# Kernel optimization log

Measured on AMD Instinct MI355X. Metric: run time of the kernel, lower is better.

The kernel has to match this reference:

```python
import jax, jax.numpy as jnp
import numpy as np

B, T = 32, 64
STOCH, DETER, HIDDEN = 1024, 4096, 1024
ACT_DIM, EMBED = 128, 1536
MIN_STD = 0.1
EPS = 1e-3  # dreamerv3-torch uses LayerNorm(eps=1e-3)


def _ln(x, g, b):
    m = jnp.mean(x, -1, keepdims=True)
    v = jnp.var(x, -1, keepdims=True)
    return (x - m) * jax.lax.rsqrt(v + EPS) * g + b


def setup_inputs() -> dict:
    key = jax.random.key(0)
    ks = jax.random.split(key, 24)

    def w(k, fan_in, fan_out):
        return jax.random.normal(k, (fan_in, fan_out), jnp.float32) / np.sqrt(fan_in)

    inp = {
        "embed": jax.random.normal(ks[0], (B, T, EMBED), jnp.float32),
        "action": jax.random.normal(ks[1], (B, T, ACT_DIM), jnp.float32),
        "is_first": jnp.zeros((B, T), jnp.bool_),
        "init_deter": jax.random.normal(ks[2], (B, DETER), jnp.float32),
        "init_stoch": jax.random.normal(ks[3], (B, STOCH), jnp.float32),
        "noise_prior": jax.random.normal(ks[4], (B, T, STOCH), jnp.float32),
        "noise_post": jax.random.normal(ks[5], (B, T, STOCH), jnp.float32),
        # _img_in_layers: Linear(stoch+act -> hidden, no bias) + LN + SiLU
        "W_in": w(ks[6], STOCH + ACT_DIM, HIDDEN),
        "g_in": 1.0 + 0.1 * jax.random.normal(ks[7], (HIDDEN,), jnp.float32),
        "b_in": 0.1 * jax.random.normal(ks[8], (HIDDEN,), jnp.float32),
        # GRUCell: Linear(hidden+deter -> 3*deter, no bias) + LN
        "W_gru": w(ks[9], HIDDEN + DETER, 3 * DETER),
        "g_gru": 1.0 + 0.1 * jax.random.normal(ks[10], (3 * DETER,), jnp.float32),
        "b_gru": 0.1 * jax.random.normal(ks[11], (3 * DETER,), jnp.float32),
        # _img_out_layers: Linear(deter -> hidden, no bias) + LN + SiLU
        "W_imgout": w(ks[12], DETER, HIDDEN),
        "g_io": 1.0 + 0.1 * jax.random.normal(ks[13], (HIDDEN,), jnp.float32),
        "b_io": 0.1 * jax.random.normal(ks[14], (HIDDEN,), jnp.float32),
        # _obs_out_layers: Linear(deter+embed -> hidden, no bias) + LN + SiLU
        "W_obsout": w(ks[15], DETER + EMBED, HIDDEN),
        "g_oo": 1.0 + 0.1 * jax.random.normal(ks[16], (HIDDEN,), jnp.float32),
        "b_oo": 0.1 * jax.random.normal(ks[17], (HIDDEN,), jnp.float32),
        # suff-stats layers: Linear(hidden -> 2*stoch) with bias
        "W_ims": w(ks[18], HIDDEN, 2 * STOCH),
        "b_ims": 0.01 * jax.random.normal(ks[19], (2 * STOCH,), jnp.float32),
        "W_obs": w(ks[20], HIDDEN, 2 * STOCH),
        "b_obs": 0.01 * jax.random.normal(ks[21], (2 * STOCH,), jnp.float32),
    }
    return inp


def _observe(embed, action, init_deter, init_stoch, noise_prior, noise_post,
             W_in, g_in, b_in, W_gru, g_gru, b_gru, W_imgout, g_io, b_io,
             W_obsout, g_oo, b_oo, W_ims, b_ims, W_obs, b_obs):
    def suff_stats(h, W, b, noise):
        stats = h @ W + b
        mean, std = jnp.split(stats, 2, -1)
        std = jax.nn.softplus(std) + MIN_STD  # std_act='softplus', mean_act='none'
        return mean, std, mean + std * noise

    def step(carry, xs):
        deter, stoch = carry
        e, a, n_p, n_q = xs
        # img_in: concat(prev_stoch, action) -> Linear -> LN -> SiLU
        x = jax.nn.silu(_ln(jnp.concatenate([stoch, a], -1) @ W_in, g_in, b_in))
        # GRUCell with layernorm (update_bias = -1)
        parts = _ln(jnp.concatenate([x, deter], -1) @ W_gru, g_gru, b_gru)
        reset, cand, update = jnp.split(parts, 3, -1)
        reset = jax.nn.sigmoid(reset)
        cand = jnp.tanh(reset * cand)
        update = jax.nn.sigmoid(update - 1.0)
        deter = update * cand + (1.0 - update) * deter
        # prior (imagination) suff stats + sample
        h_p = jax.nn.silu(_ln(deter @ W_imgout, g_io, b_io))
        mean_p, std_p, stoch_p = suff_stats(h_p, W_ims, b_ims, n_p)
        # posterior (observation) suff stats + sample
        h_q = jax.nn.silu(_ln(jnp.concatenate([deter, e], -1) @ W_obsout, g_oo, b_oo))
        mean_q, std_q, stoch_q = suff_stats(h_q, W_obs, b_obs, n_q)
        out = jnp.concatenate([deter, stoch_q, mean_q, std_q, stoch_p, mean_p, std_p], -1)
        return (deter, stoch_q), out

    xs = (jnp.swapaxes(embed, 0, 1), jnp.swapaxes(action, 0, 1),
          jnp.swapaxes(noise_prior, 0, 1), jnp.swapaxes(noise_post, 0, 1))
    _, outs = jax.lax.scan(step, (init_deter, init_stoch), xs)
    return jnp.swapaxes(outs, 0, 1)  # [B, T, deter + 6*stoch]


def reference(embed, action, is_first, init_deter, init_stoch, noise_prior, noise_post,
              W_in, g_in, b_in, W_gru, g_gru, b_gru, W_imgout, g_io, b_io,
              W_obsout, g_oo, b_oo, W_ims, b_ims, W_obs, b_obs):
    # is_first is all-False and state is given, so the init-mixing branch is never taken
    del is_first
    return _observe(embed, action, init_deter, init_stoch, noise_prior, noise_post,
                    W_in, g_in, b_in, W_gru, g_gru, b_gru, W_imgout, g_io, b_io,
                    W_obsout, g_oo, b_oo, W_ims, b_ims, W_obs, b_obs)
```

## Files before the change

kernel.cpp:

```cpp
#include <hip/hip_runtime.h>
#include <hip/hip_bf16.h>

#define T_ 64
#define DETER_ 4096
#define GRUN 12288

typedef __attribute__((ext_vector_type(8))) __bf16 bf16x8;
typedef __attribute__((ext_vector_type(4))) float f32x4;
typedef __attribute__((ext_vector_type(8))) unsigned short u16x8;
typedef __attribute__((ext_vector_type(4))) unsigned short u16x4;

__device__ inline unsigned short f2bf(float f) {
    union { float f; unsigned u; } x; x.f = f;
    unsigned r = x.u + 0x7fffu + ((x.u >> 16) & 1u);
    return (unsigned short)(r >> 16);
}
__device__ inline float sigmoidf_(float v) { return 1.f / (1.f + __expf(-v)); }
__device__ inline float siluf_(float v)    { return v / (1.f + __expf(-v)); }
__device__ inline float softplusf_(float v){ return fmaxf(v, 0.f) + __logf(1.f + __expf(-fabsf(v))); }
__device__ inline float tanhf_(float v)    { return 2.f / (1.f + __expf(-2.f * v)) - 1.f; }

__device__ inline void barrier_() {
    asm volatile("" ::: "memory");
    __builtin_amdgcn_s_barrier();
    asm volatile("" ::: "memory");
}
template <int N> __device__ inline void vmwaitN() {
    asm volatile("s_waitcnt vmcnt(%0)" :: "i"(N) : "memory");
}
__device__ inline void lgkmwait_() {
    asm volatile("s_waitcnt lgkmcnt(0)" ::: "memory");
}


__global__ __launch_bounds__(256) void k_pack(const float* __restrict__ W,
                                              unsigned short* __restrict__ dst,
                                              int K, int N) {
    long fid = (long)blockIdx.x * 256 + threadIdx.x;
    long nfr = (long)K * N / 8;
    if (fid >= nfr) return;
    int lane = (int)(fid & 63);
    long tile = fid >> 6;
    int ktiles = K >> 5;
    int k_t = (int)(tile % ktiles);
    int n_t = (int)(tile / ktiles);
    int c = lane & 15, kb = lane >> 4;
    int k0 = k_t * 32 + kb * 8;
    int n = n_t * 16 + c;
    unsigned short v[8];
#pragma unroll
    for (int i = 0; i < 8; i++) v[i] = f2bf(W[(long)(k0 + i) * N + n]);
    *reinterpret_cast<u16x8*>(dst + fid * 8) = *reinterpret_cast<u16x8*>(v);
}

__global__ __launch_bounds__(256) void k_conv(const float* __restrict__ s,
                                              unsigned short* __restrict__ d, long n) {
    long i = ((long)blockIdx.x * 256 + threadIdx.x) * 4;
    if (i >= n) return;
    f32x4 v = *reinterpret_cast<const f32x4*>(s + i);
    unsigned short o[4];
#pragma unroll
    for (int k = 0; k < 4; k++) o[k] = f2bf(v[k]);
    *reinterpret_cast<u16x4*>(d + i) = *reinterpret_cast<u16x4*>(o);
}

__global__ __launch_bounds__(256) void k_copy(const float* __restrict__ s,
                                              float* __restrict__ d, long n) {
    long i = ((long)blockIdx.x * 256 + threadIdx.x) * 4;
    if (i >= n) return;
    *reinterpret_cast<f32x4*>(d + i) = *reinterpret_cast<const f32x4*>(s + i);
}


template <int CW>
__device__ inline void stage_glds(unsigned short* chunk, const unsigned short* __restrict__ src,
                                  long ld, long k0) {
    constexpr int NI = (32 * CW * 2) / 4096;
    int wv = (int)threadIdx.x >> 6, lane = (int)threadIdx.x & 63;
#pragma unroll
    for (int i = 0; i < NI; ++i) {
        int obase = (wv * NI + i) << 10;
        int o = obase + lane * 16;
        int row = o / (CW * 2);
        int cb = o - row * (CW * 2);
        int gb = cb ^ ((row & 7) << 4);
        const char* ga = (const char*)(src + (long)row * ld + k0) + gb;
        __builtin_amdgcn_global_load_lds(
            (const __attribute__((address_space(1))) void*)ga,
            (__attribute__((address_space(3))) void*)(chunk + (obase >> 1)),
            16, 0, 0);
    }
}

__device__ inline void stage_ln512(unsigned short* chunk, const float* __restrict__ raw,
                                   int ld, int col0,
                                   const float* __restrict__ g, const float* __restrict__ b,
                                   const float* s_mean, const float* s_rstd) {
    int tid = threadIdx.x;
#pragma unroll
    for (int i = 0; i < 8; ++i) {
        int e = tid * 8 + i * 2048;
        int row = e >> 9, col = e & 511;
        float m = s_mean[row], rs = s_rstd[row];
        const float* sp = raw + (long)row * ld + col0 + col;
        unsigned short pk[8];
#pragma unroll
        for (int j = 0; j < 8; ++j) {
            float ln = (sp[j] - m) * rs * g[col0 + col + j] + b[col0 + col + j];
            pk[j] = f2bf(siluf_(ln));
        }
        int dcol = col ^ ((row & 7) << 3);
        *reinterpret_cast<u16x8*>(chunk + row * 512 + dcol) = *reinterpret_cast<u16x8*>(pk);
    }
}

__device__ inline void stage_lnsum(unsigned short* chunk, const float* __restrict__ hpart,
                                   const float* __restrict__ eprep, int t, int col0,
                                   const float* __restrict__ g, const float* __restrict__ b,
                                   const float* s_mean, const float* s_rstd) {
    int tid = threadIdx.x;
#pragma unroll
    for (int i = 0; i < 8; ++i) {
        int e = tid * 8 + i * 2048;
        int row = e >> 9, col = e & 511;
        int k = col0 + col;
        float m = s_mean[row], rs = s_rstd[row];
        const float* h0 = hpart + (long)row * 1024 + k;
        const float* ep = eprep + ((long)row * T_ + t) * 1024 + k;
        unsigned short pk[8];
#pragma unroll
        for (int jj = 0; jj < 8; jj += 4) {
            f32x4 v = *reinterpret_cast<const f32x4*>(h0 + jj);
            v += *reinterpret_cast<const f32x4*>(h0 + 32768 + jj);
            v += *reinterpret_cast<const f32x4*>(h0 + 65536 + jj);
            v += *reinterpret_cast<const f32x4*>(h0 + 98304 + jj);
            v += *reinterpret_cast<const f32x4*>(ep + jj);
#pragma unroll
            for (int j2 = 0; j2 < 4; ++j2) {
                float ln = (v[j2] - m) * rs * g[k + jj + j2] + b[k + jj + j2];
                pk[jj + j2] = f2bf(siluf_(ln));
            }
        }
        int dcol = col ^ ((row & 7) << 3);
        *reinterpret_cast<u16x8*>(chunk + row * 512 + dcol) = *reinterpret_cast<u16x8*>(pk);
    }
}

template <int CW>
__device__ inline void mfma_rh(const unsigned short* chunk, int row, int kb,
                               const unsigned short* __restrict__ bp, f32x4& acc) {
    constexpr int NKT = CW / 32;
    const unsigned short* ap = chunk + row * CW;
    int sw = (row & 7) << 3;
#pragma unroll
    for (int kt = 0; kt < NKT; ++kt) {
        bf16x8 a = *reinterpret_cast<const bf16x8*>(ap + ((kb * 8 + kt * 32) ^ sw));
        bf16x8 b = *reinterpret_cast<const bf16x8*>(bp + (long)kt * 512);
        acc = __builtin_amdgcn_mfma_f32_16x16x32_bf16(a, b, acc, 0, 0, 0);
    }
}

template <int CW>
__device__ inline void mfma2(const unsigned short* chunk, int c, int kb,
                             const unsigned short* __restrict__ bp,
                             f32x4& acc0, f32x4& acc1) {
    constexpr int NKT = CW / 32;
    const unsigned short* ap0 = chunk + c * CW;
    const unsigned short* ap1 = chunk + (16 + c) * CW;
    int sw = (c & 7) << 3;
#pragma unroll
    for (int kt = 0; kt < NKT; ++kt) {
        int off = (kb * 8 + kt * 32) ^ sw;
        bf16x8 b = *reinterpret_cast<const bf16x8*>(bp + (long)kt * 512);
        bf16x8 a0 = *reinterpret_cast<const bf16x8*>(ap0 + off);
        bf16x8 a1 = *reinterpret_cast<const bf16x8*>(ap1 + off);
        acc0 = __builtin_amdgcn_mfma_f32_16x16x32_bf16(a0, b, acc0, 0, 0, 0);
        acc1 = __builtin_amdgcn_mfma_f32_16x16x32_bf16(a1, b, acc1, 0, 0, 0);
    }
}

template <int CW, int NG, int NL>
__global__ __launch_bounds__(256) void k_gemm32(
    const unsigned short* __restrict__ Bp, int Ktiles, int ktg0,
    const unsigned short* __restrict__ srcA, long ldA,
    const float* __restrict__ lnraw, int lnld,
    const float* __restrict__ g_ln, const float* __restrict__ b_ln,
    const float* __restrict__ pstats, int nslab_in,
    const float* __restrict__ addin, long addin_ld,
    float* __restrict__ outp, long out_ld,
    float* __restrict__ partials, long prows)
{
    constexpr int NCH = NG + NL;
    constexpr int NI = (32 * CW * 2) / 4096;
    __shared__ __align__(16) unsigned short sb[2][32 * CW];
    __shared__ float s_out[32][34];
    __shared__ float s_mean[32], s_rstd[32];
    int tid = threadIdx.x;
    if (NL > 0) {
        if (tid < 32) {
            float s = 0.f, q = 0.f;
            for (int j = 0; j < nslab_in; ++j) {
                s += pstats[((long)j * 32 + tid) * 2];
                q += pstats[((long)j * 32 + tid) * 2 + 1];
            }
            float m = s * (1.f / 1024.f);
            s_mean[tid] = m;
            s_rstd[tid] = rsqrtf(q * (1.f / 1024.f) - m * m + 1e-3f);
        }
        __syncthreads();
    }
    int rowbase = blockIdx.y * 32;
    const unsigned short* srcAr = srcA + (long)rowbase * ldA;
    int lane = tid & 63, wv = tid >> 6;
    int nt = wv >> 1, rh = wv & 1;
    int c = lane & 15, kb = lane >> 4;
    int mrow = rh * 16 + c;
    long ntg = (long)blockIdx.x * 2 + nt;
    const unsigned short* bbase = Bp + (long)ntg * Ktiles * 512 + lane * 8;
    f32x4 acc = {0.f, 0.f, 0.f, 0.f};
    stage_glds<CW>(sb[0], srcAr, ldA, 0);
    for (int ch = 0; ch < NCH; ++ch) {
        int nx = ch + 1;
        if (nx < NG) stage_glds<CW>(sb[nx & 1], srcAr, ldA, (long)nx * CW);
        else if (nx < NCH) stage_ln512(sb[nx & 1], lnraw, lnld, (nx - NG) * 512,
                                       g_ln, b_ln, s_mean, s_rstd);
        if (ch < NG) { if (nx < NG) vmwaitN<NI>(); else vmwaitN<0>(); }
        if (nx >= NG && nx < NCH) lgkmwait_();
        barrier_();
        int kt0 = (ch < NG) ? (ktg0 + ch * (CW / 32)) : ((ch - NG) * 16);
        mfma_rh<CW>(sb[ch & 1], mrow, kb, bbase + (long)kt0 * 512, acc);
        barrier_();
    }
    __syncthreads();
#pragma unroll
    for (int j = 0; j < 4; ++j) s_out[rh * 16 + kb * 4 + j][nt * 16 + c] = acc[j];
    __syncthreads();
    int orow = tid >> 3, c4 = (tid & 7) * 4;
    long rg = rowbase + orow;
    float v[4]; float s = 0.f, q = 0.f;
#pragma unroll
    for (int i = 0; i < 4; ++i) {
        float x = s_out[orow][c4 + i];
        if (addin) x += addin[rg * addin_ld + blockIdx.x * 32 + c4 + i];
        v[i] = x; s += x; q += x * x;
    }
#pragma unroll
    for (int i = 0; i < 4; ++i) outp[rg * out_ld + blockIdx.x * 32 + c4 + i] = v[i];
    if (partials) {
#pragma unroll
        for (int m = 1; m < 8; m <<= 1) { s += __shfl_xor(s, m); q += __shfl_xor(q, m); }
        if ((tid & 7) == 0) {
            partials[((long)blockIdx.x * prows + rg) * 2] = s;
            partials[((long)blockIdx.x * prows + rg) * 2 + 1] = q;
        }
    }
}

__global__ __launch_bounds__(256) void k_gru2(
    const unsigned short* __restrict__ Bp,
    const unsigned short* __restrict__ deterb,
    const float* __restrict__ x_raw, const float* __restrict__ px,
    const float* __restrict__ g_in, const float* __restrict__ b_in,
    float* __restrict__ Gp0, float* __restrict__ Gp1)
{
    __shared__ __align__(16) unsigned short sb[2][32 * 512];
    __shared__ float s_out[32][66];
    __shared__ float s_mean[32], s_rstd[32];
    int tid = threadIdx.x, lane = tid & 63, wv = tid >> 6;
    int c = lane & 15, kb = lane >> 4;
    long ntg = (long)blockIdx.x * 4 + wv;
    const unsigned short* bbase = Bp + ntg * 160 * 512 + lane * 8;
    f32x4 acc0 = {0,0,0,0}, acc1 = {0,0,0,0};

    if (blockIdx.y == 0) {
        if (tid < 32) {
            float s = 0.f, q = 0.f;
            for (int j = 0; j < 32; ++j) {
                s += px[((long)j * 32 + tid) * 2];
                q += px[((long)j * 32 + tid) * 2 + 1];
            }
            float m = s * (1.f / 1024.f);
            s_mean[tid] = m;
            s_rstd[tid] = rsqrtf(q * (1.f / 1024.f) - m * m + 1e-3f);
        }
        __syncthreads();
        stage_glds<512>(sb[0], deterb, 4096, 0);
        stage_glds<512>(sb[1], deterb, 4096, 512);
        vmwaitN<8>(); barrier_();
        mfma2<512>(sb[0], c, kb, bbase + 32 * 512, acc0, acc1);
        barrier_();
        stage_glds<512>(sb[0], deterb, 4096, 1024);
        vmwaitN<8>(); barrier_();
        mfma2<512>(sb[1], c, kb, bbase + 48 * 512, acc0, acc1);
        barrier_();
        stage_ln512(sb[1], x_raw, 1024, 0, g_in, b_in, s_mean, s_rstd);
        vmwaitN<0>(); barrier_();
        mfma2<512>(sb[0], c, kb, bbase + 64 * 512, acc0, acc1);
        barrier_();
        stage_ln512(sb[0], x_raw, 1024, 512, g_in, b_in, s_mean, s_rstd);
        lgkmwait_(); barrier_();
        mfma2<512>(sb[1], c, kb, bbase + 0, acc0, acc1);
        barrier_();
        mfma2<512>(sb[0], c, kb, bbase + 16 * 512, acc0, acc1);
    } else {
        stage_glds<512>(sb[0], deterb, 4096, 1536);
        stage_glds<512>(sb[1], deterb, 4096, 2048);
        vmwaitN<8>(); barrier_();
        mfma2<512>(sb[0], c, kb, bbase + 80 * 512, acc0, acc1);
        barrier_();
        stage_glds<512>(sb[0], deterb, 4096, 2560);
        vmwaitN<8>(); barrier_();
        mfma2<512>(sb[1], c, kb, bbase + 96 * 512, acc0, acc1);
        barrier_();
        stage_glds<512>(sb[1], deterb, 4096, 3072);
        vmwaitN<8>(); barrier_();
        mfma2<512>(sb[0], c, kb, bbase + 112 * 512, acc0, acc1);
        barrier_();
        stage_glds<512>(sb[0], deterb, 4096, 3584);
        vmwaitN<8>(); barrier_();
        mfma2<512>(sb[1], c, kb, bbase + 128 * 512, acc0, acc1);
        barrier_();
        vmwaitN<0>(); barrier_();
        mfma2<512>(sb[0], c, kb, bbase + 144 * 512, acc0, acc1);
    }
    __syncthreads();
#pragma unroll
    for (int j = 0; j < 4; ++j) {
        s_out[kb * 4 + j][wv * 16 + c] = acc0[j];
        s_out[16 + kb * 4 + j][wv * 16 + c] = acc1[j];
    }
    __syncthreads();
    float* G = (blockIdx.y == 0) ? Gp0 : Gp1;
    int row = tid >> 3, c8 = (tid & 7) * 8;
#pragma unroll
    for (int i = 0; i < 8; ++i)
        G[(long)row * GRUN + blockIdx.x * 64 + c8 + i] = s_out[row][c8 + i];
}

__global__ __launch_bounds__(1024) void k_deter2(
    const float* __restrict__ Gp0, const float* __restrict__ Gp1,
    const float* __restrict__ g_gru, const float* __restrict__ b_gru,
    float* __restrict__ deterf, unsigned short* __restrict__ deterb,
    unsigned short* __restrict__ deter_allb, float* __restrict__ out, int t)
{
    __shared__ float gsh[GRUN];
    __shared__ float red[32];
    int r = blockIdx.x, tid = threadIdx.x;
    int lane = tid & 63, wv = tid >> 6;
    const float* a0 = Gp0 + (long)r * GRUN;
    const float* a1 = Gp1 + (long)r * GRUN;
    float s = 0.f, q = 0.f;
#pragma unroll
    for (int i = 0; i < 3; ++i) {
        int col = (tid + i * 1024) * 4;
        f32x4 v = *reinterpret_cast<const f32x4*>(a0 + col);
        v += *reinterpret_cast<const f32x4*>(a1 + col);
        *reinterpret_cast<f32x4*>(gsh + col) = v;
#pragma unroll
        for (int j = 0; j < 4; ++j) { s += v[j]; q += v[j] * v[j]; }
    }
#pragma unroll
    for (int m = 1; m < 64; m <<= 1) { s += __shfl_xor(s, m); q += __shfl_xor(q, m); }
    if (lane == 0) { red[wv] = s; red[16 + wv] = q; }
    __syncthreads();
    float fs = 0.f, fq = 0.f;
#pragma unroll
    for (int i = 0; i < 16; ++i) { fs += red[i]; fq += red[16 + i]; }
    float mean = fs * (1.f / 12288.f);
    float rstd = rsqrtf(fq * (1.f / 12288.f) - mean * mean + 1e-3f);
    long orow = (long)r * T_ + t;
#pragma unroll
    for (int it = 0; it < 2; ++it) {
        int j = tid * 2 + it * 2048;
        float2 rr = *reinterpret_cast<const float2*>(gsh + j);
        float2 cc = *reinterpret_cast<const float2*>(gsh + 4096 + j);
        float2 uu = *reinterpret_cast<const float2*>(gsh + 8192 + j);
        float2 dd = *reinterpret_cast<const float2*>(deterf + (long)r * DETER_ + j);
        float dn[2]; unsigned short db[2];
#pragma unroll
        for (int i = 0; i < 2; ++i) {
            float gv = (i == 0) ? rr.x : rr.y;
            float cv = (i == 0) ? cc.x : cc.y;
            float uv = (i == 0) ? uu.x : uu.y;
            float dv = (i == 0) ? dd.x : dd.y;
            float lr = (gv - mean) * rstd * g_gru[j + i] + b_gru[j + i];
            float lc = (cv - mean) * rstd * g_gru[4096 + j + i] + b_gru[4096 + j + i];
            float lu = (uv - mean) * rstd * g_gru[8192 + j + i] + b_gru[8192 + j + i];
            float reset = sigmoidf_(lr);
            float cand = tanhf_(reset * lc);
            float upd = sigmoidf_(lu - 1.f);
            dn[i] = upd * cand + (1.f - upd) * dv;
            db[i] = f2bf(dn[i]);
        }
        float2 nd; nd.x = dn[0]; nd.y = dn[1];
        *reinterpret_cast<float2*>(deterf + (long)r * DETER_ + j) = nd;
        unsigned pk = (unsigned)db[0] | ((unsigned)db[1] << 16);
        *reinterpret_cast<unsigned*>(deterb + (long)r * DETER_ + j) = pk;
        *reinterpret_cast<unsigned*>(deter_allb + orow * DETER_ + j) = pk;
        *reinterpret_cast<float2*>(out + orow * 10240 + j) = nd;
    }
}

__global__ __launch_bounds__(256) void k_h4(
    const unsigned short* __restrict__ Wood,
    const unsigned short* __restrict__ deterb,
    float* __restrict__ hpart)
{
    __shared__ __align__(16) unsigned short sb[2][32 * 512];
    __shared__ float s_out[32][66];
    int tid = threadIdx.x, lane = tid & 63, wv = tid >> 6;
    int c = lane & 15, kb = lane >> 4;
    int n = blockIdx.x, kq = blockIdx.y;
    const unsigned short* bbase = Wood + ((long)(n * 4 + wv) * 128) * 512 + lane * 8;
    f32x4 acc0 = {0,0,0,0}, acc1 = {0,0,0,0};
    stage_glds<512>(sb[0], deterb, 4096, (long)kq * 1024);
    stage_glds<512>(sb[1], deterb, 4096, (long)kq * 1024 + 512);
    vmwaitN<8>(); barrier_();
    mfma2<512>(sb[0], c, kb, bbase + (long)(kq * 32) * 512, acc0, acc1);
    vmwaitN<0>(); barrier_();
    mfma2<512>(sb[1], c, kb, bbase + (long)(kq * 32 + 16) * 512, acc0, acc1);
    __syncthreads();
#pragma unroll
    for (int j = 0; j < 4; ++j) {
        s_out[kb * 4 + j][wv * 16 + c] = acc0[j];
        s_out[16 + kb * 4 + j][wv * 16 + c] = acc1[j];
    }
    __syncthreads();
    int row = tid >> 3, c8 = (tid & 7) * 8;
    float* hp = hpart + (long)kq * 32768 + (long)row * 1024 + n * 64 + c8;
#pragma unroll
    for (int i = 0; i < 8; ++i) hp[i] = s_out[row][c8 + i];
}

__global__ __launch_bounds__(256) void k_statsq2(
    const unsigned short* __restrict__ Bp, const float* __restrict__ hpart,
    const float* __restrict__ E_pre,
    const float* __restrict__ g_oo, const float* __restrict__ b_oo,
    const float* __restrict__ bias,
    const float* __restrict__ noise, float* __restrict__ out,
    unsigned short* __restrict__ stochb, int t)
{
    __shared__ __align__(16) unsigned short sb[2][32 * 512];
    __shared__ float s_out[32][66];
    __shared__ float s_mean[32], s_rstd[32];
    int tid = threadIdx.x, lane = tid & 63, wv = tid >> 6;
    int c = lane & 15, kb = lane >> 4;
    {
        int row = tid >> 3, c0 = (tid & 7) * 128;
        const float* h0 = hpart + (long)row * 1024 + c0;
        const float* ep = E_pre + ((long)row * T_ + t) * 1024 + c0;
        float s = 0.f, q = 0.f;
#pragma unroll 8
        for (int kk = 0; kk < 128; kk += 4) {
            f32x4 v = *reinterpret_cast<const f32x4*>(h0 + kk);
            v += *reinterpret_cast<const f32x4*>(h0 + 32768 + kk);
            v += *reinterpret_cast<const f32x4*>(h0 + 65536 + kk);
            v += *reinterpret_cast<const f32x4*>(h0 + 98304 + kk);
            v += *reinterpret_cast<const f32x4*>(ep + kk);
#pragma unroll
            for (int j2 = 0; j2 < 4; ++j2) { s += v[j2]; q += v[j2] * v[j2]; }
        }
#pragma unroll
        for (int m = 1; m < 8; m <<= 1) { s += __shfl_xor(s, m); q += __shfl_xor(q, m); }
        if ((tid & 7) == 0) {
            float mm = s * (1.f / 1024.f);
            s_mean[row] = mm;
            s_rstd[row] = rsqrtf(q * (1.f / 1024.f) - mm * mm + 1e-3f);
        }
    }
    __syncthreads();
    int part = wv >> 1, nt = wv & 1;
    long ntg = (long)part * 64 + blockIdx.x * 2 + nt;
    const unsigned short* bbase = Bp + ntg * 32 * 512 + lane * 8;
    f32x4 acc0 = {0,0,0,0}, acc1 = {0,0,0,0};
    stage_lnsum(sb[0], hpart, E_pre, t, 0, g_oo, b_oo, s_mean, s_rstd);
    stage_lnsum(sb[1], hpart, E_pre, t, 512, g_oo, b_oo, s_mean, s_rstd);
    lgkmwait_(); barrier_();
    mfma2<512>(sb[0], c, kb, bbase, acc0, acc1);
    mfma2<512>(sb[1], c, kb, bbase + 16 * 512, acc0, acc1);
    __syncthreads();
    float bv = bias[ntg * 16 + c];
#pragma unroll
    for (int j = 0; j < 4; ++j) {
        s_out[kb * 4 + j][part * 32 + nt * 16 + c] = acc0[j] + bv;
        s_out[16 + kb * 4 + j][part * 32 + nt * 16 + c] = acc1[j] + bv;
    }
    __syncthreads();
    int r = tid >> 3, j0 = (tid & 7) * 4;
    long orow = (long)r * T_ + t;
#pragma unroll
    for (int i = 0; i < 4; ++i) {
        int j = j0 + i;
        float mean = s_out[r][j];
        float sd = softplusf_(s_out[r][32 + j]) + 0.1f;
        int cg2 = blockIdx.x * 32 + j;
        float st = mean + sd * noise[orow * 1024 + cg2];
        float* op = out + orow * 10240;
        op[4096 + cg2] = st; op[5120 + cg2] = mean; op[6144 + cg2] = sd;
        stochb[(long)r * 1024 + cg2] = f2bf(st);
    }
}

__global__ __launch_bounds__(256) void k_bstats(
    const unsigned short* __restrict__ Bp, const unsigned short* __restrict__ h_pb,
    const float* __restrict__ bias, const float* __restrict__ noise,
    float* __restrict__ out)
{
    __shared__ __align__(16) unsigned short sb[2][32 * 512];
    __shared__ float s_out[32][66];
    int tid = threadIdx.x;
    int lane = tid & 63, wv = tid >> 6;
    int part = wv >> 1, nt = wv & 1;
    int c = lane & 15, kb = lane >> 4;
    int s_ = blockIdx.x, rowbase = blockIdx.y * 32;
    const unsigned short* A = h_pb + (long)rowbase * 1024;
    long ntg = (long)part * 64 + s_ * 2 + nt;
    const unsigned short* bbase = Bp + ntg * 32 * 512 + lane * 8;
    f32x4 acc0 = {0.f,0.f,0.f,0.f}, acc1 = {0.f,0.f,0.f,0.f};
    stage_glds<512>(sb[0], A, 1024, 0);
    stage_glds<512>(sb[1], A, 1024, 512);
    vmwaitN<8>(); barrier_();
    mfma_rh<512>(sb[0], c, kb, bbase, acc0);
    mfma_rh<512>(sb[0], 16 + c, kb, bbase, acc1);
    vmwaitN<0>(); barrier_();
    mfma_rh<512>(sb[1], c, kb, bbase + 16 * 512, acc0);
    mfma_rh<512>(sb[1], 16 + c, kb, bbase + 16 * 512, acc1);
    __syncthreads();
    float bv = bias[ntg * 16 + c];
#pragma unroll
    for (int j = 0; j < 4; ++j) {
        s_out[kb * 4 + j][part * 32 + nt * 16 + c] = acc0[j] + bv;
        s_out[16 + kb * 4 + j][part * 32 + nt * 16 + c] = acc1[j] + bv;
    }
    __syncthreads();
    int r = tid >> 3, j0 = (tid & 7) * 4;
    long orow = rowbase + r;
#pragma unroll
    for (int i = 0; i < 4; ++i) {
        int j = j0 + i;
        float mean = s_out[r][j];
        float sd = softplusf_(s_out[r][32 + j]) + 0.1f;
        int cg2 = s_ * 32 + j;
        float st = mean + sd * noise[orow * 1024 + cg2];
        float* op = out + orow * 10240;
        op[7168 + cg2] = st; op[8192 + cg2] = mean; op[9216 + cg2] = sd;
    }
}

__global__ __launch_bounds__(256) void k_bfin(const float* __restrict__ hp_raw,
                                              const float* __restrict__ pbh,
                                              const float* __restrict__ g_io,
                                              const float* __restrict__ b_io,
                                              unsigned short* __restrict__ h_pb) {
    int row = blockIdx.x * 8 + ((int)threadIdx.x >> 5);
    int l = threadIdx.x & 31;
    float s = pbh[((long)l * 2048 + row) * 2];
    float q = pbh[((long)l * 2048 + row) * 2 + 1];
#pragma unroll
    for (int m = 16; m; m >>= 1) { s += __shfl_xor(s, m, 32); q += __shfl_xor(q, m, 32); }
    float mn = s * (1.f / 1024.f);
    float rs = rsqrtf(q * (1.f / 1024.f) - mn * mn + 1e-3f);
#pragma unroll
    for (int i = 0; i < 8; ++i) {
        int col = i * 128 + l * 4;
        f32x4 v = *reinterpret_cast<const f32x4*>(hp_raw + (long)row * 1024 + col);
        unsigned short pk[4];
#pragma unroll
        for (int j = 0; j < 4; ++j) {
            float ln = (v[j] - mn) * rs * g_io[col + j] + b_io[col + j];
            pk[j] = f2bf(siluf_(ln));
        }
        *reinterpret_cast<u16x4*>(h_pb + (long)row * 1024 + col) = *reinterpret_cast<u16x4*>(pk);
    }
}


extern "C" void kernel_launch(void* const* d_in, const int* in_sizes, int n_in,
                              void* d_out, int out_size, void* d_ws, size_t ws_size,
                              hipStream_t stream) {
    const float* embed      = (const float*)d_in[0];
    const float* action     = (const float*)d_in[1];
    const float* init_deter = (const float*)d_in[3];
    const float* init_stoch = (const float*)d_in[4];
    const float* noise_pr   = (const float*)d_in[5];
    const float* noise_po   = (const float*)d_in[6];
    const float* W_in       = (const float*)d_in[7];
    const float* g_in       = (const float*)d_in[8];
    const float* b_in       = (const float*)d_in[9];
    const float* W_gru      = (const float*)d_in[10];
    const float* g_gru      = (const float*)d_in[11];
    const float* b_gru      = (const float*)d_in[12];
    const float* W_io       = (const float*)d_in[13];
    const float* g_io       = (const float*)d_in[14];
    const float* b_io       = (const float*)d_in[15];
    const float* W_oo       = (const float*)d_in[16];
    const float* g_oo       = (const float*)d_in[17];
    const float* b_oo       = (const float*)d_in[18];
    const float* W_ims      = (const float*)d_in[19];
    const float* b_ims      = (const float*)d_in[20];
    const float* W_obs      = (const float*)d_in[21];
    const float* b_obs      = (const float*)d_in[22];
    float* out = (float*)d_out;

    char* ws = (char*)d_ws;
    size_t off = 0;
    auto alloc = [&](size_t bytes) {
        size_t r = off;
        off = (off + bytes + 255) & ~(size_t)255;
        return r;
    };
    unsigned short* pWgru  = (unsigned short*)(ws + alloc((size_t)5120 * 12288 * 2));
    unsigned short* pWin_s = (unsigned short*)(ws + alloc((size_t)1024 * 1024 * 2));
    unsigned short* pWin_a = (unsigned short*)(ws + alloc((size_t)128 * 1024 * 2));
    unsigned short* pWio   = (unsigned short*)(ws + alloc((size_t)4096 * 1024 * 2));
    unsigned short* pWood  = (unsigned short*)(ws + alloc((size_t)4096 * 1024 * 2));
    unsigned short* pWooe  = (unsigned short*)(ws + alloc((size_t)1536 * 1024 * 2));
    unsigned short* pWims  = (unsigned short*)(ws + alloc((size_t)1024 * 2048 * 2));
    unsigned short* pWobs  = (unsigned short*)(ws + alloc((size_t)1024 * 2048 * 2));
    unsigned short* act_bf = (unsigned short*)(ws + alloc((size_t)2048 * 128 * 2));
    unsigned short* emb_bf = (unsigned short*)(ws + alloc((size_t)2048 * 1536 * 2));
    float* A_pre  = (float*)(ws + alloc((size_t)2048 * 1024 * 4));
    float* E_pre  = (float*)(ws + alloc((size_t)2048 * 1024 * 4));
    float* x_raw  = (float*)(ws + alloc((size_t)32 * 1024 * 4));
    float* Gp0    = (float*)(ws + alloc((size_t)32 * GRUN * 4));
    float* Gp1    = (float*)(ws + alloc((size_t)32 * GRUN * 4));
    float* deterf = (float*)(ws + alloc((size_t)32 * DETER_ * 4));
    unsigned short* deterb     = (unsigned short*)(ws + alloc((size_t)32 * DETER_ * 2));
    unsigned short* deter_allb = (unsigned short*)(ws + alloc((size_t)2048 * DETER_ * 2));
    unsigned short* stochb = (unsigned short*)(ws + alloc((size_t)32 * 1024 * 2));
    float* hp_raw = (float*)(ws + alloc((size_t)2048 * 1024 * 4));
    unsigned short* h_pb = (unsigned short*)(ws + alloc((size_t)2048 * 1024 * 2));
    float* px  = (float*)(ws + alloc((size_t)32 * 32 * 2 * 4));
    float* pbh = (float*)(ws + alloc((size_t)32 * 2048 * 2 * 4));
    float* hpart = (float*)(ws + alloc((size_t)4 * 32 * 1024 * 4));
    (void)ws_size; (void)out_size; (void)n_in; (void)in_sizes;

    auto packgrid = [](long K, long N) { return (unsigned)((K * N / 8 + 255) / 256); };

    k_pack<<<packgrid(5120, 12288), 256, 0, stream>>>(W_gru, pWgru, 5120, 12288);
    k_pack<<<packgrid(1024, 1024), 256, 0, stream>>>(W_in, pWin_s, 1024, 1024);
    k_pack<<<packgrid(128, 1024), 256, 0, stream>>>(W_in + (size_t)1024 * 1024, pWin_a, 128, 1024);
    k_pack<<<packgrid(4096, 1024), 256, 0, stream>>>(W_io, pWio, 4096, 1024);
    k_pack<<<packgrid(4096, 1024), 256, 0, stream>>>(W_oo, pWood, 4096, 1024);
    k_pack<<<packgrid(1536, 1024), 256, 0, stream>>>(W_oo + (size_t)4096 * 1024, pWooe, 1536, 1024);
    k_pack<<<packgrid(1024, 2048), 256, 0, stream>>>(W_ims, pWims, 1024, 2048);
    k_pack<<<packgrid(1024, 2048), 256, 0, stream>>>(W_obs, pWobs, 1024, 2048);
    k_conv<<<(2048 * 128 / 4 + 255) / 256, 256, 0, stream>>>(action, act_bf, 2048L * 128);
    k_conv<<<(2048 * 1536 / 4 + 255) / 256, 256, 0, stream>>>(embed, emb_bf, 2048L * 1536);
    k_conv<<<(32 * 1024 / 4 + 255) / 256, 256, 0, stream>>>(init_stoch, stochb, 32L * 1024);
    k_conv<<<(32 * 4096 / 4 + 255) / 256, 256, 0, stream>>>(init_deter, deterb, 32L * 4096);
    k_copy<<<(32 * 4096 / 4 + 255) / 256, 256, 0, stream>>>(init_deter, deterf, 32L * 4096);
    k_gemm32<128, 1, 0><<<dim3(32, 64), 256, 0, stream>>>(
        pWin_a, 4, 0, act_bf, 128, nullptr, 0, nullptr, nullptr, nullptr, 0,
        nullptr, 0, A_pre, 1024, nullptr, 0);
    k_gemm32<512, 3, 0><<<dim3(32, 64), 256, 0, stream>>>(
        pWooe, 48, 0, emb_bf, 1536, nullptr, 0, nullptr, nullptr, nullptr, 0,
        nullptr, 0, E_pre, 1024, nullptr, 0);

    for (int t = 0; t < T_; ++t) {
        k_gemm32<512, 2, 0><<<dim3(32, 1), 256, 0, stream>>>(
            pWin_s, 32, 0, stochb, 1024, nullptr, 0, nullptr, nullptr, nullptr, 0,
            A_pre + (size_t)t * 1024, (long)T_ * 1024, x_raw, 1024, px, 32);
        k_gru2<<<dim3(192, 2), 256, 0, stream>>>(pWgru, deterb, x_raw, px, g_in, b_in,
                                                 Gp0, Gp1);
        k_deter2<<<32, 1024, 0, stream>>>(Gp0, Gp1, g_gru, b_gru, deterf, deterb,
                                          deter_allb, out, t);
        k_h4<<<dim3(16, 4), 256, 0, stream>>>(pWood, deterb, hpart);
        k_statsq2<<<32, 256, 0, stream>>>(pWobs, hpart, E_pre, g_oo, b_oo, b_obs,
                                          noise_po, out, stochb, t);
    }

    k_gemm32<512, 8, 0><<<dim3(32, 64), 256, 0, stream>>>(
        pWio, 128, 0, deter_allb, 4096, nullptr, 0, nullptr, nullptr, nullptr, 0,
        nullptr, 0, hp_raw, 1024, pbh, 2048);
    k_bfin<<<256, 256, 0, stream>>>(hp_raw, pbh, g_io, b_io, h_pb);
    k_bstats<<<dim3(32, 64), 256, 0, stream>>>(pWims, h_pb, b_ims, noise_pr, out);
}
```

Measured before the change: 7.000 ms.

## Split GRU GEMM K dimension four ways with smaller double-buffered chunks

The per-step GRU GEMM now splits the K=5120 reduction across four blocks in y instead of two, giving 768 blocks rather than 384. LDS staging chunks shrink from 512 to 256 columns, and launch bounds request three blocks per CU. The goal is more parallelism and occupancy to better hide weight streaming latency in this memory-bound step. In exchange, the deter kernel must read and sum four partial buffers, which adds global traffic for the partials.

```diff
diff --git a/kernel.cpp b/kernel.cpp
--- a/kernel.cpp
+++ b/kernel.cpp
@@ -111,6 +111,28 @@
         }
         int dcol = col ^ ((row & 7) << 3);
         *reinterpret_cast<u16x8*>(chunk + row * 512 + dcol) = *reinterpret_cast<u16x8*>(pk);
+    }
+}
+
+__device__ inline void stage_ln256(unsigned short* chunk, const float* __restrict__ raw,
+                                   int ld, int col0,
+                                   const float* __restrict__ g, const float* __restrict__ b,
+                                   const float* s_mean, const float* s_rstd) {
+    int tid = threadIdx.x;
+#pragma unroll
+    for (int i = 0; i < 4; ++i) {
+        int e = tid * 8 + i * 2048;
+        int row = e >> 8, col = e & 255;
+        float m = s_mean[row], rs = s_rstd[row];
+        const float* sp = raw + (long)row * ld + col0 + col;
+        unsigned short pk[8];
+#pragma unroll
+        for (int j = 0; j < 8; ++j) {
+            float ln = (sp[j] - m) * rs * g[col0 + col + j] + b[col0 + col + j];
+            pk[j] = f2bf(siluf_(ln));
+        }
+        int dcol = col ^ ((row & 7) << 3);
+        *reinterpret_cast<u16x8*>(chunk + row * 256 + dcol) = *reinterpret_cast<u16x8*>(pk);
     }
 }
 
@@ -256,23 +278,24 @@
     }
 }
 
-__global__ __launch_bounds__(256) void k_gru2(
+__global__ __launch_bounds__(256, 3) void k_gru4(
     const unsigned short* __restrict__ Bp,
     const unsigned short* __restrict__ deterb,
     const float* __restrict__ x_raw, const float* __restrict__ px,
     const float* __restrict__ g_in, const float* __restrict__ b_in,
-    float* __restrict__ Gp0, float* __restrict__ Gp1)
+    float* __restrict__ Gp)
 {
-    __shared__ __align__(16) unsigned short sb[2][32 * 512];
+    __shared__ __align__(16) unsigned short sb[2][32 * 256];
     __shared__ float s_out[32][66];
     __shared__ float s_mean[32], s_rstd[32];
     int tid = threadIdx.x, lane = tid & 63, wv = tid >> 6;
     int c = lane & 15, kb = lane >> 4;
+    int kq = blockIdx.y;
     long ntg = (long)blockIdx.x * 4 + wv;
-    const unsigned short* bbase = Bp + ntg * 160 * 512 + lane * 8;
-    f32x4 acc0 = {0,0,0,0}, acc1 = {0,0,0,0};
-
-    if (blockIdx.y == 0) {
+    const unsigned short* bb = Bp + ntg * 160 * 512 + lane * 8;
+    f32x4 acc0 = {0, 0, 0, 0}, acc1 = {0, 0, 0, 0};
+
+    if (kq == 0) {
         if (tid < 32) {
             float s = 0.f, q = 0.f;
             for (int j = 0; j < 32; ++j) {
@@ -284,44 +307,31 @@
             s_rstd[tid] = rsqrtf(q * (1.f / 1024.f) - m * m + 1e-3f);
         }
         __syncthreads();
-        stage_glds<512>(sb[0], deterb, 4096, 0);
-        stage_glds<512>(sb[1], deterb, 4096, 512);
-        vmwaitN<8>(); barrier_();
-        mfma2<512>(sb[0], c, kb, bbase + 32 * 512, acc0, acc1);
-        barrier_();
-        stage_glds<512>(sb[0], deterb, 4096, 1024);
-        vmwaitN<8>(); barrier_();
-        mfma2<512>(sb[1], c, kb, bbase + 48 * 512, acc0, acc1);
-        barrier_();
-        stage_ln512(sb[1], x_raw, 1024, 0, g_in, b_in, s_mean, s_rstd);
-        vmwaitN<0>(); barrier_();
-        mfma2<512>(sb[0], c, kb, bbase + 64 * 512, acc0, acc1);
-        barrier_();
-        stage_ln512(sb[0], x_raw, 1024, 512, g_in, b_in, s_mean, s_rstd);
-        lgkmwait_(); barrier_();
-        mfma2<512>(sb[1], c, kb, bbase + 0, acc0, acc1);
-        barrier_();
-        mfma2<512>(sb[0], c, kb, bbase + 16 * 512, acc0, acc1);
+        stage_ln256(sb[0], x_raw, 1024, 0, g_in, b_in, s_mean, s_rstd);
+        stage_ln256(sb[1], x_raw, 1024, 256, g_in, b_in, s_mean, s_rstd);
+#pragma unroll
+        for (int ch = 0; ch < 4; ++ch) {
+            lgkmwait_(); barrier_();
+            mfma2<256>(sb[ch & 1], c, kb, bb + (long)(8 * ch) * 512, acc0, acc1);
+            barrier_();
+            if (ch + 2 < 4)
+                stage_ln256(sb[ch & 1], x_raw, 1024, 256 * (ch + 2), g_in, b_in,
+                            s_mean, s_rstd);
+        }
     } else {
-        stage_glds<512>(sb[0], deterb, 4096, 1536);
-        stage_glds<512>(sb[1], deterb, 4096, 2048);
-        vmwaitN<8>(); barrier_();
-        mfma2<512>(sb[0], c, kb, bbase + 80 * 512, acc0, acc1);
-        barrier_();
-        stage_glds<512>(sb[0], deterb, 4096, 2560);
-        vmwaitN<8>(); barrier_();
-        mfma2<512>(sb[1], c, kb, bbase + 96 * 512, acc0, acc1);
-        barrier_();
-        stage_glds<512>(sb[1], deterb, 4096, 3072);
-        vmwaitN<8>(); barrier_();
-        mfma2<512>(sb[0], c, kb, bbase + 112 * 512, acc0, acc1);
-        barrier_();
-        stage_glds<512>(sb[0], deterb, 4096, 3584);
-        vmwaitN<8>(); barrier_();
-        mfma2<512>(sb[1], c, kb, bbase + 128 * 512, acc0, acc1);
-        barrier_();
-        vmwaitN<0>(); barrier_();
-        mfma2<512>(sb[0], c, kb, bbase + 144 * 512, acc0, acc1);
+        int nch = (kq == 3) ? 6 : 5;
+        long o0 = (kq == 1) ? 0 : (kq == 2 ? 1280 : 2560);
+        int kt0 = (kq == 1) ? 32 : (kq == 2 ? 72 : 112);
+        stage_glds<256>(sb[0], deterb, 4096, o0);
+        stage_glds<256>(sb[1], deterb, 4096, o0 + 256);
+        for (int ch = 0; ch < nch; ++ch) {
+            if (ch < nch - 1) vmwaitN<4>(); else vmwaitN<0>();
+            barrier_();
+            mfma2<256>(sb[ch & 1], c, kb, bb + (long)(kt0 + 8 * ch) * 512, acc0, acc1);
+            barrier_();
+            if (ch + 2 < nch)
+                stage_glds<256>(sb[ch & 1], deterb, 4096, o0 + 256 * (ch + 2));
+        }
     }
     __syncthreads();
 #pragma unroll
@@ -330,15 +340,14 @@
         s_out[16 + kb * 4 + j][wv * 16 + c] = acc1[j];
     }
     __syncthreads();
-    float* G = (blockIdx.y == 0) ? Gp0 : Gp1;
     int row = tid >> 3, c8 = (tid & 7) * 8;
-#pragma unroll
-    for (int i = 0; i < 8; ++i)
-        G[(long)row * GRUN + blockIdx.x * 64 + c8 + i] = s_out[row][c8 + i];
-}
-
-__global__ __launch_bounds__(1024) void k_deter2(
-    const float* __restrict__ Gp0, const float* __restrict__ Gp1,
+    float* G = Gp + (long)kq * 32 * GRUN + (long)row * GRUN + blockIdx.x * 64 + c8;
+#pragma unroll
+    for (int i = 0; i < 8; ++i) G[i] = s_out[row][c8 + i];
+}
+
+__global__ __launch_bounds__(1024) void k_deter4(
+    const float* __restrict__ Gp,
     const float* __restrict__ g_gru, const float* __restrict__ b_gru,
     float* __restrict__ deterf, unsigned short* __restrict__ deterb,
     unsigned short* __restrict__ deter_allb, float* __restrict__ out, int t)
@@ -347,14 +356,15 @@
     __shared__ float red[32];
     int r = blockIdx.x, tid = threadIdx.x;
     int lane = tid & 63, wv = tid >> 6;
-    const float* a0 = Gp0 + (long)r * GRUN;
-    const float* a1 = Gp1 + (long)r * GRUN;
+    const float* g0 = Gp + (long)r * GRUN;
     float s = 0.f, q = 0.f;
 #pragma unroll
     for (int i = 0; i < 3; ++i) {
         int col = (tid + i * 1024) * 4;
-        f32x4 v = *reinterpret_cast<const f32x4*>(a0 + col);
-        v += *reinterpret_cast<const f32x4*>(a1 + col);
+        f32x4 v = *reinterpret_cast<const f32x4*>(g0 + col);
+        v += *reinterpret_cast<const f32x4*>(g0 + 393216 + col);
+        v += *reinterpret_cast<const f32x4*>(g0 + 786432 + col);
+        v += *reinterpret_cast<const f32x4*>(g0 + 1179648 + col);
         *reinterpret_cast<f32x4*>(gsh + col) = v;
 #pragma unroll
         for (int j = 0; j < 4; ++j) { s += v[j]; q += v[j] * v[j]; }
@@ -622,8 +632,7 @@
     float* A_pre  = (float*)(ws + alloc((size_t)2048 * 1024 * 4));
     float* E_pre  = (float*)(ws + alloc((size_t)2048 * 1024 * 4));
     float* x_raw  = (float*)(ws + alloc((size_t)32 * 1024 * 4));
-    float* Gp0    = (float*)(ws + alloc((size_t)32 * GRUN * 4));
-    float* Gp1    = (float*)(ws + alloc((size_t)32 * GRUN * 4));
+    float* Gp     = (float*)(ws + alloc((size_t)4 * 32 * GRUN * 4));
     float* deterf = (float*)(ws + alloc((size_t)32 * DETER_ * 4));
     unsigned short* deterb     = (unsigned short*)(ws + alloc((size_t)32 * DETER_ * 2));
     unsigned short* deter_allb = (unsigned short*)(ws + alloc((size_t)2048 * DETER_ * 2));
@@ -661,9 +670,8 @@
         k_gemm32<512, 2, 0><<<dim3(32, 1), 256, 0, stream>>>(
             pWin_s, 32, 0, stochb, 1024, nullptr, 0, nullptr, nullptr, nullptr, 0,
             A_pre + (size_t)t * 1024, (long)T_ * 1024, x_raw, 1024, px, 32);
-        k_gru2<<<dim3(192, 2), 256, 0, stream>>>(pWgru, deterb, x_raw, px, g_in, b_in,
-                                                 Gp0, Gp1);
-        k_deter2<<<32, 1024, 0, stream>>>(Gp0, Gp1, g_gru, b_gru, deterf, deterb,
+        k_gru4<<<dim3(192, 4), 256, 0, stream>>>(pWgru, deterb, x_raw, px, g_in, b_in, Gp);
+        k_deter4<<<32, 1024, 0, stream>>>(Gp, g_gru, b_gru, deterf, deterb,
                                           deter_allb, out, t);
         k_h4<<<dim3(16, 4), 256, 0, stream>>>(pWood, deterb, hpart);
         k_statsq2<<<32, 256, 0, stream>>>(pWobs, hpart, E_pre, g_oo, b_oo, b_obs,
```

Result: faster. 5.984 ms (median of 3 runs) (-14.5%).
